# Kernel optimization log

Hardware: AMD Instinct MI355X
Metric: run time of the kernel (lower is better)

Reference implementation:

```python
import jax, jax.numpy as jnp
import numpy as np

K = 3            # kernel_size
FILTERS = 256
GC = 16          # group_channels (hardcoded in module)
G = FILTERS // GC  # groups = 16


def setup_inputs() -> dict:
    key = jax.random.key(0)
    ks = jax.random.split(key, 5)
    B, H, W, C = 8, 64, 64, FILTERS
    red = FILTERS // 4  # reduction_ratio = 4
    x = jax.random.normal(ks[0], (B, H, W, C), dtype=jnp.float32)
    W1 = jax.random.normal(ks[1], (C, red), dtype=jnp.float32) * 0.05
    b1 = jnp.zeros((red,), dtype=jnp.float32)
    W2 = jax.random.normal(ks[2], (red, K * K * G), dtype=jnp.float32) * 0.05
    b2 = jnp.zeros((K * K * G,), dtype=jnp.float32)
    return {"x": x, "W1": W1, "b1": b1, "W2": W2, "b2": b2}


def reference(x, W1, b1, W2, b2):
    b, h, w, c = x.shape
    kk = K * K
    # kernel generator: two 1x1 convs (note: norm1/relu1 are defined but unused in the original call())
    wgt = jnp.einsum('bhwc,cd->bhwd', x, W1) + b1          # [b,h,w,c/4]
    wgt = jnp.einsum('bhwd,de->bhwe', wgt, W2) + b2        # [b,h,w,kk*G]
    # transpose to channel-first, reshape (b, G, kk, h, w), expand group-channel dim
    wgt = wgt.transpose(0, 3, 1, 2).reshape(b, G, 1, kk, h, w)
    # SAME-padded 3x3 patch extraction, stride 1; TF depth layout is (ki, kj, c)
    pad = (K - 1) // 2
    xp = jnp.pad(x, ((0, 0), (pad, K - 1 - pad), (pad, K - 1 - pad), (0, 0)))
    patches = jnp.stack([xp[:, i:i + h, j:j + w, :] for i in range(K) for j in range(K)], axis=3)  # [b,h,w,kk,c]
    # replicate TF's transpose + row-major reshape of the (kk*c) flat dim into (G, GC, kk)
    out = patches.reshape(b, h, w, kk * c).transpose(0, 3, 1, 2).reshape(b, G, GC, kk, h, w)
    out = jnp.einsum('bgokhw,bgckhw->bgchw', wgt, out)     # multiply + reduce over kk
    out = out.reshape(b, FILTERS, h, w).transpose(0, 2, 3, 1)
    return out
```

## Files before the change

kernel.cpp:

```cpp
#include <hip/hip_runtime.h>

namespace {
constexpr int XP = 264;
constexpr int XR = 18 * XP;
constexpr int EWP = 148;

typedef _Float16 h2 __attribute__((ext_vector_type(2)));
typedef _Float16 h8 __attribute__((ext_vector_type(8)));
typedef float f32x4 __attribute__((ext_vector_type(4)));

__device__ __forceinline__ h2 pkrtz(float a, float b) {
  return __builtin_bit_cast(h2, __builtin_amdgcn_cvt_pkrtz(a, b));
}

#if __has_builtin(__builtin_amdgcn_fdot2)
#define HAS_FDOT2 1
#else
#define HAS_FDOT2 0
#endif

__global__ __launch_bounds__(256) void prep_w12(
    const float* __restrict__ W1, const float* __restrict__ b1,
    const float* __restrict__ W2, const float* __restrict__ b2,
    _Float16* __restrict__ pack, float* __restrict__ b12)
{
  __shared__ float sW1[256 * 66];
  const int t = threadIdx.x, e = blockIdx.x;
#pragma unroll
  for (int j = 0; j < 32; ++j) {
    int idx = (j * 256 + t) * 2;
    int c = idx >> 6, d = idx & 63;
    float2 v = *(const float2*)(W1 + idx);
    *(float2*)(&sW1[c * 66 + d]) = v;
  }
  __syncthreads();
  const int c = t;
  float acc = 0.f;
  for (int d = 0; d < 64; ++d)
    acc += sW1[c * 66 + d] * W2[d * 144 + e];
  int T = e >> 4, n = e & 15;
  int s = c >> 5, q = (c >> 3) & 3, j = c & 7;
  pack[(((T * 8 + s) * 64 + q * 16 + n) << 3) + j] = (_Float16)acc;
  if (t == 0) {
    float bb = b2[e];
    for (int d = 0; d < 64; ++d) bb += b1[d] * W2[d * 144 + e];
    b12[e] = bb;
  }
}

__global__ __launch_bounds__(256) void invo_fused(
    const float* __restrict__ x,
    const _Float16* __restrict__ pack,
    const float* __restrict__ b12g,
    float* __restrict__ out)
{
  __shared__ __align__(16) _Float16 xg[3 * XR];
  __shared__ float ew[16 * EWP];

  const int t = threadIdx.x;
  const int blk = blockIdx.x;
  const int strip = blk & 3;
  const int bh = blk >> 2;
  const int h = bh & 63;
  const int b = bh >> 6;
  const int w0 = strip * 16;

  for (int idx = t; idx < 3 * 18 * 64; idx += 256) {
    int c4 = (idx & 63) << 2;
    int pr = idx >> 6;
    int r = (pr >= 36) ? 2 : (pr >= 18 ? 1 : 0);
    int j = pr - r * 18;
    int hh = h + r - 1, ww = w0 + j - 1;
    float4 v = make_float4(0.f, 0.f, 0.f, 0.f);
    if (((unsigned)hh < 64u) && ((unsigned)ww < 64u))
      v = *(const float4*)(x + ((((b << 6) + hh) << 6) + ww) * 256 + c4);
    h2 lo = pkrtz(v.x, v.y);
    h2 hi = pkrtz(v.z, v.w);
    uint2 u;
    u.x = __builtin_bit_cast(unsigned, lo);
    u.y = __builtin_bit_cast(unsigned, hi);
    *(uint2*)(&xg[r * XR + j * XP + c4]) = u;
  }
  __syncthreads();

  {
    const int wave = t >> 6, lane = t & 63;
    const int q = lane >> 4, m = lane & 15;
    h8 A[8];
    const _Float16* arow = &xg[XR + (m + 1) * XP + q * 8];
#pragma unroll
    for (int s = 0; s < 8; ++s)
      A[s] = *(const h8*)(arow + s * 32);
    for (int T = wave; T < 9; T += 4) {
      f32x4 acc = {0.f, 0.f, 0.f, 0.f};
      const h8* bp = (const h8*)pack + (T * 8) * 64 + lane;
#pragma unroll
      for (int s = 0; s < 8; ++s)
        acc = __builtin_amdgcn_mfma_f32_16x16x32_f16(A[s], bp[s * 64], acc, 0, 0, 0);
      float bb = b12g[T * 16 + m];
#pragma unroll
      for (int r = 0; r < 4; ++r)
        ew[(q * 4 + r) * EWP + T * 16 + m] = acc[r] + bb;
    }
  }
  __syncthreads();

  {
    const int p = t >> 4, g = t & 15;
    float ewr[9];
#pragma unroll
    for (int k = 0; k < 9; ++k) ewr[k] = ew[p * EWP + g * 9 + k];
    h2 wp[8];
#pragma unroll
    for (int m = 0; m < 8; ++m)
      wp[m] = pkrtz(ewr[m], ewr[m + 1]);
    const float w8 = ewr[8], wb0 = ewr[0];
    const int g144 = g * 144;
    const int pbase = p * XP;
    float res[16];
#pragma unroll
    for (int gc = 0; gc < 16; ++gc) res[gc] = 0.f;
#pragma unroll
    for (int j = 0; j < 18; ++j) {
      int f = g144 + j * 8;
      int tap = f >> 8;
      int ch = f & 255;
      int di = (tap * 86) >> 8;
      int dj = tap - 3 * di;
      uint4 dv = *(const uint4*)(&xg[di * XR + (p + dj) * XP + ch]);
      h2 v[4];
      v[0] = __builtin_bit_cast(h2, dv.x);
      v[1] = __builtin_bit_cast(h2, dv.y);
      v[2] = __builtin_bit_cast(h2, dv.z);
      v[3] = __builtin_bit_cast(h2, dv.w);
#pragma unroll
      for (int i = 0; i < 4; ++i) {
        const int u = j * 8 + 2 * i;
        const int m = u % 9;
        if (m == 8) {
          res[u / 9]     += (float)v[i][0] * w8;
          res[u / 9 + 1] += (float)v[i][1] * wb0;
        } else {
#if HAS_FDOT2
          res[u / 9] = __builtin_amdgcn_fdot2(v[i], wp[m], res[u / 9], false);
#else
          res[u / 9] += (float)v[i][0] * ewr[m] + (float)v[i][1] * ewr[m + 1];
#endif
        }
      }
    }
    float* orow = out + (size_t)(((((b << 6) + h) << 6) + w0 + p)) * 256 + (g << 4);
    *(float4*)(orow + 0)  = make_float4(res[0],  res[1],  res[2],  res[3]);
    *(float4*)(orow + 4)  = make_float4(res[4],  res[5],  res[6],  res[7]);
    *(float4*)(orow + 8)  = make_float4(res[8],  res[9],  res[10], res[11]);
    *(float4*)(orow + 12) = make_float4(res[12], res[13], res[14], res[15]);
  }
}
}

extern "C" void kernel_launch(void* const* d_in, const int* in_sizes, int n_in,
                              void* d_out, int out_size, void* d_ws, size_t ws_size,
                              hipStream_t stream) {
  const float* x  = (const float*)d_in[0];
  const float* W1 = (const float*)d_in[1];
  const float* b1 = (const float*)d_in[2];
  const float* W2 = (const float*)d_in[3];
  const float* b2 = (const float*)d_in[4];
  float* out = (float*)d_out;
  _Float16* pack = (_Float16*)d_ws;
  float* b12 = (float*)((char*)d_ws + 9 * 8 * 64 * 8 * 2);
  prep_w12<<<144, 256, 0, stream>>>(W1, b1, W2, b2, pack, b12);
  invo_fused<<<8 * 64 * 4, 256, 0, stream>>>(x, pack, b12, out);
}
```

Before: 117.9 us.

## Split kernel-generator GEMM into separate kernel writing fp16 weights to workspace

Moves the per-pixel 256->144 weight GEMM out of the fused involution kernel into its own kernel. That kernel processes 64 pixels per block with all four waves busy on MFMA, and writes fp16 weights to a workspace buffer. The involution kernel then loads those precomputed weights instead of running the GEMM with only some waves active (T = wave; T < 9; T += 4, so waves 1-3 get 2 tiles and wave 0 gets 3). The cost is an extra kernel launch, an extra global round trip of about 9 MB of fp16 weights, and a second read of x. The old fused path is kept as a fallback when the workspace is too small.

Result: slower. 140.5 us (+19.1%).

```diff
diff --git a/kernel.cpp b/kernel.cpp
--- a/kernel.cpp
+++ b/kernel.cpp
@@ -4,6 +4,7 @@
 constexpr int XP = 264;
 constexpr int XR = 18 * XP;
 constexpr int EWP = 148;
+constexpr int ETP = 152;
 
 typedef _Float16 h2 __attribute__((ext_vector_type(2)));
 typedef _Float16 h8 __attribute__((ext_vector_type(8)));
@@ -48,10 +49,63 @@
   }
 }
 
-__global__ __launch_bounds__(256) void invo_fused(
-    const float* __restrict__ x,
-    const _Float16* __restrict__ pack,
-    const float* __restrict__ b12g,
+__global__ __launch_bounds__(256) void egemm(
+    const float* __restrict__ x, const _Float16* __restrict__ pack,
+    const float* __restrict__ b12g, _Float16* __restrict__ ebuf)
+{
+  __shared__ __align__(16) _Float16 xs[64 * XP];
+  const int t = threadIdx.x;
+  const int px0 = blockIdx.x * 64;
+  const float* xrow = x + (size_t)px0 * 256;
+
+#pragma unroll
+  for (int j = 0; j < 16; ++j) {
+    int idx = j * 256 + t;
+    int p = idx >> 6, c4 = (idx & 63) << 2;
+    float4 v = *(const float4*)(xrow + (idx << 2));
+    h2 lo = pkrtz(v.x, v.y), hi = pkrtz(v.z, v.w);
+    uint2 u;
+    u.x = __builtin_bit_cast(unsigned, lo);
+    u.y = __builtin_bit_cast(unsigned, hi);
+    *(uint2*)(&xs[p * XP + c4]) = u;
+  }
+  __syncthreads();
+
+  const int wave = t >> 6, lane = t & 63;
+  const int q = lane >> 4, m = lane & 15;
+  h8 A[8];
+  const _Float16* arow = &xs[(wave * 16 + m) * XP + q * 8];
+#pragma unroll
+  for (int s = 0; s < 8; ++s) A[s] = *(const h8*)(arow + s * 32);
+  __syncthreads();
+
+  _Float16* et = xs;
+  for (int T = 0; T < 9; ++T) {
+    f32x4 acc = {0.f, 0.f, 0.f, 0.f};
+    const h8* bp = (const h8*)pack + (T * 8) * 64 + lane;
+#pragma unroll
+    for (int s = 0; s < 8; ++s)
+      acc = __builtin_amdgcn_mfma_f32_16x16x32_f16(A[s], bp[s * 64], acc, 0, 0, 0);
+    float bb = b12g[T * 16 + m];
+#pragma unroll
+    for (int r = 0; r < 4; ++r)
+      et[(wave * 16 + q * 4 + r) * ETP + T * 16 + m] = (_Float16)(acc[r] + bb);
+  }
+  __syncthreads();
+
+#pragma unroll
+  for (int j = 0; j < 5; ++j) {
+    int idx = j * 256 + t;
+    if (idx < 1152) {
+      int p = idx / 18, cc = idx % 18;
+      uint4 v = *(const uint4*)(&et[p * ETP + cc * 8]);
+      *(uint4*)(ebuf + (size_t)(px0 + p) * 144 + cc * 8) = v;
+    }
+  }
+}
+
+__global__ __launch_bounds__(256) void invo(
+    const float* __restrict__ x, const _Float16* __restrict__ ebuf,
     float* __restrict__ out)
 {
   __shared__ __align__(16) _Float16 xg[3 * XR];
@@ -64,6 +118,7 @@
   const int h = bh & 63;
   const int b = bh >> 6;
   const int w0 = strip * 16;
+  const int pix0 = ((b << 6) + h) * 64 + w0;
 
   for (int idx = t; idx < 3 * 18 * 64; idx += 256) {
     int c4 = (idx & 63) << 2;
@@ -74,23 +129,111 @@
     float4 v = make_float4(0.f, 0.f, 0.f, 0.f);
     if (((unsigned)hh < 64u) && ((unsigned)ww < 64u))
       v = *(const float4*)(x + ((((b << 6) + hh) << 6) + ww) * 256 + c4);
-    h2 lo = pkrtz(v.x, v.y);
-    h2 hi = pkrtz(v.z, v.w);
+    h2 lo = pkrtz(v.x, v.y), hi = pkrtz(v.z, v.w);
     uint2 u;
     u.x = __builtin_bit_cast(unsigned, lo);
     u.y = __builtin_bit_cast(unsigned, hi);
     *(uint2*)(&xg[r * XR + j * XP + c4]) = u;
   }
-  __syncthreads();
-
+  for (int idx = t; idx < 288; idx += 256) {
+    int p = idx / 18, cc = idx % 18;
+    uint4 v = *(const uint4*)(ebuf + (size_t)(pix0 + p) * 144 + cc * 8);
+    h2 e0 = __builtin_bit_cast(h2, v.x), e1 = __builtin_bit_cast(h2, v.y);
+    h2 e2 = __builtin_bit_cast(h2, v.z), e3 = __builtin_bit_cast(h2, v.w);
+    float* dst = &ew[p * EWP + cc * 8];
+    *(float4*)(dst + 0) = make_float4((float)e0[0], (float)e0[1], (float)e1[0], (float)e1[1]);
+    *(float4*)(dst + 4) = make_float4((float)e2[0], (float)e2[1], (float)e3[0], (float)e3[1]);
+  }
+  __syncthreads();
+
+  {
+    const int p = t >> 4, g = t & 15;
+    float ewr[9];
+#pragma unroll
+    for (int k = 0; k < 9; ++k) ewr[k] = ew[p * EWP + g * 9 + k];
+    h2 wp[8];
+#pragma unroll
+    for (int m = 0; m < 8; ++m)
+      wp[m] = pkrtz(ewr[m], ewr[m + 1]);
+    const float w8 = ewr[8], wb0 = ewr[0];
+    const int g144 = g * 144;
+    const int pbase = p * XP;
+    float res[16];
+#pragma unroll
+    for (int gc = 0; gc < 16; ++gc) res[gc] = 0.f;
+#pragma unroll
+    for (int j = 0; j < 18; ++j) {
+      int f = g144 + j * 8;
+      int tap = f >> 8;
+      int ch = f & 255;
+      int di = (tap * 86) >> 8;
+      int dj = tap - 3 * di;
+      uint4 dv = *(const uint4*)(&xg[di * XR + (p + dj) * XP + ch]);
+      h2 v[4];
+      v[0] = __builtin_bit_cast(h2, dv.x);
+      v[1] = __builtin_bit_cast(h2, dv.y);
+      v[2] = __builtin_bit_cast(h2, dv.z);
+      v[3] = __builtin_bit_cast(h2, dv.w);
+#pragma unroll
+      for (int i = 0; i < 4; ++i) {
+        const int u = j * 8 + 2 * i;
+        const int m = u % 9;
+        if (m == 8) {
+          res[u / 9]     += (float)v[i][0] * w8;
+          res[u / 9 + 1] += (float)v[i][1] * wb0;
+        } else {
+#if HAS_FDOT2
+          res[u / 9] = __builtin_amdgcn_fdot2(v[i], wp[m], res[u / 9], false);
+#else
+          res[u / 9] += (float)v[i][0] * ewr[m] + (float)v[i][1] * ewr[m + 1];
+#endif
+        }
+      }
+    }
+    float* orow = out + (size_t)(pix0 + p) * 256 + (g << 4);
+    *(float4*)(orow + 0)  = make_float4(res[0],  res[1],  res[2],  res[3]);
+    *(float4*)(orow + 4)  = make_float4(res[4],  res[5],  res[6],  res[7]);
+    *(float4*)(orow + 8)  = make_float4(res[8],  res[9],  res[10], res[11]);
+    *(float4*)(orow + 12) = make_float4(res[12], res[13], res[14], res[15]);
+  }
+}
+
+__global__ __launch_bounds__(256) void invo_fused(
+    const float* __restrict__ x, const _Float16* __restrict__ pack,
+    const float* __restrict__ b12g, float* __restrict__ out)
+{
+  __shared__ __align__(16) _Float16 xg[3 * XR];
+  __shared__ float ew[16 * EWP];
+  const int t = threadIdx.x;
+  const int blk = blockIdx.x;
+  const int strip = blk & 3;
+  const int bh = blk >> 2;
+  const int h = bh & 63;
+  const int b = bh >> 6;
+  const int w0 = strip * 16;
+  for (int idx = t; idx < 3 * 18 * 64; idx += 256) {
+    int c4 = (idx & 63) << 2;
+    int pr = idx >> 6;
+    int r = (pr >= 36) ? 2 : (pr >= 18 ? 1 : 0);
+    int j = pr - r * 18;
+    int hh = h + r - 1, ww = w0 + j - 1;
+    float4 v = make_float4(0.f, 0.f, 0.f, 0.f);
+    if (((unsigned)hh < 64u) && ((unsigned)ww < 64u))
+      v = *(const float4*)(x + ((((b << 6) + hh) << 6) + ww) * 256 + c4);
+    h2 lo = pkrtz(v.x, v.y), hi = pkrtz(v.z, v.w);
+    uint2 u;
+    u.x = __builtin_bit_cast(unsigned, lo);
+    u.y = __builtin_bit_cast(unsigned, hi);
+    *(uint2*)(&xg[r * XR + j * XP + c4]) = u;
+  }
+  __syncthreads();
   {
     const int wave = t >> 6, lane = t & 63;
     const int q = lane >> 4, m = lane & 15;
     h8 A[8];
     const _Float16* arow = &xg[XR + (m + 1) * XP + q * 8];
 #pragma unroll
-    for (int s = 0; s < 8; ++s)
-      A[s] = *(const h8*)(arow + s * 32);
+    for (int s = 0; s < 8; ++s) A[s] = *(const h8*)(arow + s * 32);
     for (int T = wave; T < 9; T += 4) {
       f32x4 acc = {0.f, 0.f, 0.f, 0.f};
       const h8* bp = (const h8*)pack + (T * 8) * 64 + lane;
@@ -104,7 +247,6 @@
     }
   }
   __syncthreads();
-
   {
     const int p = t >> 4, g = t & 15;
     float ewr[9];
@@ -112,8 +254,7 @@
     for (int k = 0; k < 9; ++k) ewr[k] = ew[p * EWP + g * 9 + k];
     h2 wp[8];
 #pragma unroll
-    for (int m = 0; m < 8; ++m)
-      wp[m] = pkrtz(ewr[m], ewr[m + 1]);
+    for (int m = 0; m < 8; ++m) wp[m] = pkrtz(ewr[m], ewr[m + 1]);
     const float w8 = ewr[8], wb0 = ewr[0];
     const int g144 = g * 144;
     const int pbase = p * XP;
@@ -168,7 +309,15 @@
   const float* b2 = (const float*)d_in[4];
   float* out = (float*)d_out;
   _Float16* pack = (_Float16*)d_ws;
-  float* b12 = (float*)((char*)d_ws + 9 * 8 * 64 * 8 * 2);
+  float* b12 = (float*)((char*)d_ws + 73728);
+  const size_t EOFF = 131072;
+  const size_t ENEED = EOFF + (size_t)32768 * 144 * 2;
   prep_w12<<<144, 256, 0, stream>>>(W1, b1, W2, b2, pack, b12);
-  invo_fused<<<8 * 64 * 4, 256, 0, stream>>>(x, pack, b12, out);
-}
+  if (ws_size >= ENEED) {
+    _Float16* ebuf = (_Float16*)((char*)d_ws + EOFF);
+    egemm<<<512, 256, 0, stream>>>(x, pack, b12, ebuf);
+    invo<<<2048, 256, 0, stream>>>(x, ebuf, out);
+  } else {
+    invo_fused<<<2048, 256, 0, stream>>>(x, pack, b12, out);
+  }
+}
```
